# Kernel optimization log

Hardware: AMD Instinct MI355X
Metric: run time of the kernel (lower is better)

The kernel has to match this reference:

```python
import jax, jax.numpy as jnp
import numpy as np

D_MODEL = 2048
D_KV = 512
D_Q = 1536
N_HEADS = 16
HEAD_DIM = 128
ROPE_BASE = 10000.0


def apply_rope(x, past_len=0):
    # x: [B, H, S, D]; interleaved-pair rotation (pairs (2i, 2i+1))
    B, H, S, D = x.shape
    half = D // 2
    pos = (jnp.arange(S) + past_len).astype(jnp.float32)
    inv_freq = 1.0 / (ROPE_BASE ** (jnp.arange(half, dtype=jnp.float32) * 2.0 / D))
    ang = pos[:, None] * inv_freq[None, :]          # [S, half]
    cos, sin = jnp.cos(ang), jnp.sin(ang)
    x1 = x[..., 0::2]
    x2 = x[..., 1::2]
    r1 = x1 * cos - x2 * sin
    r2 = x1 * sin + x2 * cos
    return jnp.stack([r1, r2], axis=-1).reshape(x.shape)


def setup_inputs() -> dict:
    key = jax.random.key(0)
    ks = jax.random.split(key, 16)
    s = 0.02
    inp = {
        "h": jax.random.normal(ks[0], (2, 2048, D_MODEL), dtype=jnp.float32),
        # weights stored [in, out] (y = x @ W + b)
        "W_DKV": jax.random.normal(ks[1], (D_MODEL, D_KV)) * s,
        "b_DKV": jnp.zeros((D_KV,)),
        "W_UK": jax.random.normal(ks[2], (D_KV, N_HEADS * HEAD_DIM)) * s,
        "b_UK": jnp.zeros((N_HEADS * HEAD_DIM,)),
        "W_UV": jax.random.normal(ks[3], (D_KV, N_HEADS * HEAD_DIM)) * s,
        "b_UV": jnp.zeros((N_HEADS * HEAD_DIM,)),
        "W_DQ": jax.random.normal(ks[4], (D_MODEL, D_Q)) * s,
        "b_DQ": jnp.zeros((D_Q,)),
        "W_UQ": jax.random.normal(ks[5], (D_Q, N_HEADS * HEAD_DIM)) * s,
        "b_UQ": jnp.zeros((N_HEADS * HEAD_DIM,)),
        "W_KR": jax.random.normal(ks[6], (D_MODEL, D_MODEL)) * s,
        "b_KR": jnp.zeros((D_MODEL,)),
        "W_O": jax.random.normal(ks[7], (D_MODEL, D_MODEL)) * s,
        "b_O": jnp.zeros((D_MODEL,)),
    }
    return inp


def reference(h, W_DKV, b_DKV, W_UK, b_UK, W_UV, b_UV, W_DQ, b_DQ,
              W_UQ, b_UQ, W_KR, b_KR, W_O, b_O):
    B, S, _ = h.shape

    def split_heads(x):  # [B,S,H*D] -> [B,H,S,D]
        return x.reshape(B, S, N_HEADS, HEAD_DIM).transpose(0, 2, 1, 3)

    # latent KV path (prefill: no cache)
    c_KV = h @ W_DKV + b_DKV                     # [B,S,d_kv] latent cache
    k_C = split_heads(c_KV @ W_UK + b_UK)        # [B,H,S,Dh]
    v_C = split_heads(c_KV @ W_UV + b_UV)        # [B,H,S,Dh]

    # decoupled RoPE K path
    kr_cache = h @ W_KR + b_KR                   # [B,S,d_model]
    k_R = apply_rope(split_heads(kr_cache))      # [B,H,S,Dh]
    k = jnp.concatenate([k_C, k_R], axis=-1)     # [B,H,S,2*Dh]

    # latent Q path
    c_Q = h @ W_DQ + b_DQ
    q_C = split_heads(c_Q @ W_UQ + b_UQ)
    q_R = apply_rope(q_C, past_len=0)
    q = jnp.concatenate([q_C, q_R], axis=-1)     # [B,H,S,2*Dh]

    # causal attention
    scale = 1.0 / jnp.sqrt(jnp.float32(q.shape[-1]))
    scores = jnp.einsum("bhqd,bhkd->bhqk", q, k) * scale
    causal = jnp.tril(jnp.ones((S, S), dtype=bool))
    scores = jnp.where(causal, scores, jnp.finfo(scores.dtype).min)
    attn = jax.nn.softmax(scores, axis=-1)
    ctx = jnp.einsum("bhqk,bhkd->bhqd", attn, v_C)
    ctx = ctx.transpose(0, 2, 1, 3).reshape(B, S, N_HEADS * HEAD_DIM)
    out = ctx @ W_O + b_O
    return (out, c_KV, kr_cache)
```

## Files before the change

kernel.cpp:

```cpp
#include <hip/hip_runtime.h>
#include <cstdint>
#include <cstddef>

typedef __bf16 bf16;
typedef __bf16 bf16x8 __attribute__((ext_vector_type(8)));
typedef float  f32x4  __attribute__((ext_vector_type(4)));

__device__ __forceinline__ void async_copy16(const void* g, void* l)
{
    auto gp = (__attribute__((address_space(1))) const void*)(reinterpret_cast<uintptr_t>(g));
    auto lp = (__attribute__((address_space(3))) void*)(uint32_t)(reinterpret_cast<uintptr_t>(l));
    __builtin_amdgcn_global_load_lds(gp, lp, 16, 0, 0);
}

__global__ void cast_to_bf16(const float* __restrict__ in, bf16* __restrict__ out, int n)
{
    const int i = (blockIdx.x * 256 + threadIdx.x) * 4;
    if (i < n) {
        const float4 v = *(const float4*)(in + i);
        out[i]     = (bf16)v.x;
        out[i + 1] = (bf16)v.y;
        out[i + 2] = (bf16)v.z;
        out[i + 3] = (bf16)v.w;
    }
}

__global__ void transpose_cast(const float* __restrict__ in, bf16* __restrict__ out,
                               int R, int Ccols)
{
    __shared__ float tile[32][33];
    const int c0 = blockIdx.x * 32;
    const int r0 = blockIdx.y * 32;
    const int tx = threadIdx.x, ty = threadIdx.y;
    for (int i = ty; i < 32; i += 8)
        tile[i][tx] = in[(size_t)(r0 + i) * Ccols + c0 + tx];
    __syncthreads();
    for (int i = ty; i < 32; i += 8)
        out[(size_t)(c0 + i) * R + r0 + tx] = (bf16)tile[tx][i];
}

__global__ __launch_bounds__(256, 2)
void gemm_bt(const bf16* __restrict__ A, const bf16* __restrict__ Bt,
             const float* __restrict__ bias, float* __restrict__ C,
             bf16* __restrict__ Cb, int M, int N, int K)
{
    __shared__ bf16 As[128 * 64];
    __shared__ bf16 Bs[128 * 64];
    const int tid  = threadIdx.x;
    const int wave = tid >> 6;
    const int lane = tid & 63;
    const int quad = lane >> 4;
    const int l15  = lane & 15;
    const int m0   = blockIdx.y * 128;
    const int n0   = blockIdx.x * 128;
    const int wm   = (wave >> 1) * 64;
    const int wn   = (wave & 1) * 64;

    const int srow = lane >> 3;
    const int scol = (lane & 7) * 8;
    const bf16* Ab = A  + (size_t)(m0 + wave * 32 + srow) * K + scol;
    const bf16* Bb = Bt + (size_t)(n0 + wave * 32 + srow) * K + scol;
    bf16* AsW = &As[(wave * 32) * 64];
    bf16* BsW = &Bs[(wave * 32) * 64];

    f32x4 acc[4][4] = {};

    for (int k0 = 0; k0 < K; k0 += 64) {
        __syncthreads();
#pragma unroll
        for (int i = 0; i < 4; ++i) {
            async_copy16(Ab + (size_t)(i * 8) * K + k0, AsW + i * 8 * 64);
            async_copy16(Bb + (size_t)(i * 8) * K + k0, BsW + i * 8 * 64);
        }
        __syncthreads();
#pragma unroll
        for (int ks = 0; ks < 2; ++ks) {
            bf16x8 af[4], bfr[4];
#pragma unroll
            for (int i = 0; i < 4; ++i)
                af[i] = *(const bf16x8*)&As[(wm + i * 16 + l15) * 64 + ks * 32 + quad * 8];
#pragma unroll
            for (int j = 0; j < 4; ++j)
                bfr[j] = *(const bf16x8*)&Bs[(wn + j * 16 + l15) * 64 + ks * 32 + quad * 8];
#pragma unroll
            for (int i = 0; i < 4; ++i)
#pragma unroll
                for (int j = 0; j < 4; ++j)
                    acc[i][j] = __builtin_amdgcn_mfma_f32_16x16x32_bf16(af[i], bfr[j], acc[i][j], 0, 0, 0);
        }
    }

#pragma unroll
    for (int j = 0; j < 4; ++j) {
        const int col = n0 + wn + j * 16 + l15;
        const float bv = bias[col];
#pragma unroll
        for (int i = 0; i < 4; ++i) {
            const int row = m0 + wm + i * 16 + quad * 4;
#pragma unroll
            for (int r = 0; r < 4; ++r) {
                const float v = acc[i][j][r] + bv;
                if (C)  C [(size_t)(row + r) * N + col] = v;
                if (Cb) Cb[(size_t)(row + r) * N + col] = (bf16)v;
            }
        }
    }
}

__global__ void transpose_v(const bf16* __restrict__ vC, bf16* __restrict__ vT)
{
    __shared__ bf16 tile[32][33];
    const int bh = blockIdx.z, b = bh >> 4, h = bh & 15;
    const int s0 = blockIdx.x * 32, d0 = blockIdx.y * 32;
    const int tx = threadIdx.x, ty = threadIdx.y;
    for (int i = ty; i < 32; i += 8)
        tile[i][tx] = vC[((size_t)(b * 2048 + s0 + i)) * 2048 + h * 128 + d0 + tx];
    __syncthreads();
    for (int i = ty; i < 32; i += 8)
        vT[((size_t)(bh * 128 + d0 + i)) * 2048 + s0 + tx] = tile[tx][i];
}

#define INVF_C 0.20762050593046014f

template <typename T>
__global__ void rope_heads(const T* __restrict__ in, bf16* __restrict__ out)
{
    const int idx = blockIdx.x * 256 + threadIdx.x;
    const int j = idx & 63;
    const int h = (idx >> 6) & 15;
    const int s = (idx >> 10) & 2047;
    const int b = idx >> 21;
    const size_t src = ((size_t)(b * 2048 + s)) * 2048 + h * 128 + 2 * j;
    const float x1 = (float)in[src], x2 = (float)in[src + 1];
    const float ang = (float)s * exp2f(-(float)j * INVF_C);
    float sn, cs;
    sincosf(ang, &sn, &cs);
    out[src]     = (bf16)(x1 * cs - x2 * sn);
    out[src + 1] = (bf16)(x1 * sn + x2 * cs);
}

__global__ __launch_bounds__(512, 2)
void mla_attn(const bf16* __restrict__ qCp, const bf16* __restrict__ qRp,
              const bf16* __restrict__ kCp, const bf16* __restrict__ kRp,
              const bf16* __restrict__ Vt, bf16* __restrict__ ctx)
{
    __shared__ bf16 Ks[64 * 264];
    __shared__ bf16 Vs[128 * 72];
    __shared__ bf16 Ps[128 * 72];
    const int bh   = blockIdx.x;
    const int b    = bh >> 4, hh = bh & 15;
    const int yq   = blockIdx.y;
    const int qt   = (yq < 8) ? (2 * yq) : (31 - 2 * yq);
    const int q0   = qt * 128;
    const int tid  = threadIdx.x;
    const int wave = tid >> 6;
    const int lane = tid & 63;
    const int quad = lane >> 4;
    const int l15  = lane & 15;
    const int wq   = q0 + wave * 16;

    bf16x8 qf[8];
    {
        const size_t qoff = ((size_t)(b * 2048 + wq + l15)) * 2048
                          + hh * 128 + quad * 8;
#pragma unroll
        for (int ks = 0; ks < 4; ++ks) {
            qf[ks]     = *(const bf16x8*)(qCp + qoff + ks * 32);
            qf[4 + ks] = *(const bf16x8*)(qRp + qoff + ks * 32);
        }
    }

    float mstate[4], lstate[4];
    f32x4 o[8];
#pragma unroll
    for (int r = 0; r < 4; ++r) { mstate[r] = -1e30f; lstate[r] = 0.0f; }
#pragma unroll
    for (int dt = 0; dt < 8; ++dt) { f32x4 z = {0.f, 0.f, 0.f, 0.f}; o[dt] = z; }

    const int krow = tid >> 4, kcol = (tid & 15) * 8;
    const int vsr  = tid >> 3, vsc  = (tid & 7) * 8;

    const int ntiles = 2 * qt + 2;
    for (int t = 0; t < ntiles; ++t) {
        const int kk0 = t * 64;
        __syncthreads();
#pragma unroll
        for (int it = 0; it < 2; ++it) {
            const int row = it * 32 + krow;
            const size_t g = ((size_t)(b * 2048 + kk0 + row)) * 2048 + hh * 128 + kcol;
            *(bf16x8*)&Ks[row * 264 + kcol]       = *(const bf16x8*)(kCp + g);
            *(bf16x8*)&Ks[row * 264 + 128 + kcol] = *(const bf16x8*)(kRp + g);
        }
#pragma unroll
        for (int it = 0; it < 2; ++it) {
            const int d = it * 64 + vsr;
            *(bf16x8*)&Vs[d * 72 + vsc] =
                *(const bf16x8*)(Vt + ((size_t)(bh * 128 + d)) * 2048 + kk0 + vsc);
        }
        __syncthreads();

        if (kk0 <= wq + 15) {
            f32x4 sc[4] = {};
#pragma unroll
            for (int ks = 0; ks < 8; ++ks)
#pragma unroll
                for (int j = 0; j < 4; ++j) {
                    bf16x8 kf = *(const bf16x8*)&Ks[(j * 16 + l15) * 264 + ks * 32 + quad * 8];
                    sc[j] = __builtin_amdgcn_mfma_f32_16x16x32_bf16(qf[ks], kf, sc[j], 0, 0, 0);
                }

            const bool diag = (kk0 + 63 > wq);
            float rowmax[4] = {-1e30f, -1e30f, -1e30f, -1e30f};
#pragma unroll
            for (int j = 0; j < 4; ++j) {
                const int kkcol = kk0 + j * 16 + l15;
#pragma unroll
                for (int r = 0; r < 4; ++r) {
                    float s = sc[j][r] * 0.0625f;
                    if (diag && (kkcol > wq + quad * 4 + r)) s = -1e30f;
                    sc[j][r] = s;
                    rowmax[r] = fmaxf(rowmax[r], s);
                }
            }
#pragma unroll
            for (int r = 0; r < 4; ++r) {
                float v = rowmax[r];
                v = fmaxf(v, __shfl_xor(v, 1, 64));
                v = fmaxf(v, __shfl_xor(v, 2, 64));
                v = fmaxf(v, __shfl_xor(v, 4, 64));
                v = fmaxf(v, __shfl_xor(v, 8, 64));
                rowmax[r] = v;
            }
            float alpha[4];
#pragma unroll
            for (int r = 0; r < 4; ++r) {
                const float mnew = fmaxf(mstate[r], rowmax[r]);
                alpha[r] = __expf(mstate[r] - mnew);
                mstate[r] = mnew;
            }
            float rowsum[4] = {0.f, 0.f, 0.f, 0.f};
#pragma unroll
            for (int j = 0; j < 4; ++j)
#pragma unroll
                for (int r = 0; r < 4; ++r) {
                    const float p = __expf(sc[j][r] - mstate[r]);
                    sc[j][r] = p;
                    rowsum[r] += p;
                }
#pragma unroll
            for (int r = 0; r < 4; ++r) {
                float v = rowsum[r];
                v += __shfl_xor(v, 1, 64);
                v += __shfl_xor(v, 2, 64);
                v += __shfl_xor(v, 4, 64);
                v += __shfl_xor(v, 8, 64);
                lstate[r] = lstate[r] * alpha[r] + v;
            }
#pragma unroll
            for (int j = 0; j < 4; ++j)
#pragma unroll
                for (int r = 0; r < 4; ++r)
                    Ps[(wave * 16 + quad * 4 + r) * 72 + j * 16 + l15] = (bf16)sc[j][r];
#pragma unroll
            for (int dt = 0; dt < 8; ++dt)
#pragma unroll
                for (int r = 0; r < 4; ++r)
                    o[dt][r] *= alpha[r];
#pragma unroll
            for (int ks2 = 0; ks2 < 2; ++ks2) {
                bf16x8 pf = *(const bf16x8*)&Ps[(wave * 16 + l15) * 72 + ks2 * 32 + quad * 8];
#pragma unroll
                for (int dt = 0; dt < 8; ++dt) {
                    bf16x8 vf = *(const bf16x8*)&Vs[(dt * 16 + l15) * 72 + ks2 * 32 + quad * 8];
                    o[dt] = __builtin_amdgcn_mfma_f32_16x16x32_bf16(pf, vf, o[dt], 0, 0, 0);
                }
            }
        }
    }

    float inv_l[4];
#pragma unroll
    for (int r = 0; r < 4; ++r) inv_l[r] = 1.0f / lstate[r];
#pragma unroll
    for (int dt = 0; dt < 8; ++dt) {
        const int d = dt * 16 + l15;
#pragma unroll
        for (int r = 0; r < 4; ++r) {
            const int q = wq + quad * 4 + r;
            ctx[((size_t)(b * 2048 + q)) * 2048 + hh * 128 + d] = (bf16)(o[dt][r] * inv_l[r]);
        }
    }
}

extern "C" void kernel_launch(void* const* d_in, const int* in_sizes, int n_in,
                              void* d_out, int out_size, void* d_ws, size_t ws_size,
                              hipStream_t stream)
{
    const float* h     = (const float*)d_in[0];
    const float* W_DKV = (const float*)d_in[1];
    const float* b_DKV = (const float*)d_in[2];
    const float* W_UK  = (const float*)d_in[3];
    const float* b_UK  = (const float*)d_in[4];
    const float* W_UV  = (const float*)d_in[5];
    const float* b_UV  = (const float*)d_in[6];
    const float* W_DQ  = (const float*)d_in[7];
    const float* b_DQ  = (const float*)d_in[8];
    const float* W_UQ  = (const float*)d_in[9];
    const float* b_UQ  = (const float*)d_in[10];
    const float* W_KR  = (const float*)d_in[11];
    const float* b_KR  = (const float*)d_in[12];
    const float* W_O   = (const float*)d_in[13];
    const float* b_O   = (const float*)d_in[14];

    float* out   = (float*)d_out;
    float* cKV_f = out + (size_t)8388608;
    float* krc_f = out + (size_t)10485760;

    bf16* vT = (bf16*)d_out;
    bf16* qR = (bf16*)d_out + 8388608;

    bf16* ws   = (bf16*)d_ws;
    bf16* hb   = ws + 0;
    bf16* Wt   = ws + 8388608;
    bf16* cKVb = ws + 12582912;
    bf16* kC   = ws + 14680064;
    bf16* vC   = ws + 23068672;
    bf16* cQ   = ws + 31457280;
    bf16* qC   = ws + 37748736;
    bf16* kR   = hb;
    bf16* ctx  = vC;

    dim3 tb(32, 8);

    cast_to_bf16<<<8192, 256, 0, stream>>>(h, hb, 8388608);

    transpose_cast<<<dim3(16, 64), tb, 0, stream>>>(W_DKV, Wt, 2048, 512);
    gemm_bt<<<dim3(4, 32),  256, 0, stream>>>(hb, Wt, b_DKV, cKV_f, cKVb, 4096, 512,  2048);

    transpose_cast<<<dim3(64, 64), tb, 0, stream>>>(W_KR, Wt, 2048, 2048);
    gemm_bt<<<dim3(16, 32), 256, 0, stream>>>(hb, Wt, b_KR, krc_f, nullptr, 4096, 2048, 2048);

    transpose_cast<<<dim3(48, 64), tb, 0, stream>>>(W_DQ, Wt, 2048, 1536);
    gemm_bt<<<dim3(12, 32), 256, 0, stream>>>(hb, Wt, b_DQ, nullptr, cQ, 4096, 1536, 2048);

    transpose_cast<<<dim3(64, 16), tb, 0, stream>>>(W_UK, Wt, 512, 2048);
    gemm_bt<<<dim3(16, 32), 256, 0, stream>>>(cKVb, Wt, b_UK, nullptr, kC, 4096, 2048, 512);

    transpose_cast<<<dim3(64, 16), tb, 0, stream>>>(W_UV, Wt, 512, 2048);
    gemm_bt<<<dim3(16, 32), 256, 0, stream>>>(cKVb, Wt, b_UV, nullptr, vC, 4096, 2048, 512);

    transpose_cast<<<dim3(64, 48), tb, 0, stream>>>(W_UQ, Wt, 1536, 2048);
    gemm_bt<<<dim3(16, 32), 256, 0, stream>>>(cQ, Wt, b_UQ, nullptr, qC, 4096, 2048, 1536);

    rope_heads<float><<<16384, 256, 0, stream>>>(krc_f, kR);
    rope_heads<bf16 ><<<16384, 256, 0, stream>>>(qC, qR);
    transpose_v<<<dim3(64, 4, 32), tb, 0, stream>>>(vC, vT);

    mla_attn<<<dim3(32, 16), 512, 0, stream>>>(qC, qR, kC, kR, vT, ctx);

    transpose_cast<<<dim3(64, 64), tb, 0, stream>>>(W_O, Wt, 2048, 2048);
    gemm_bt<<<dim3(16, 32), 256, 0, stream>>>(ctx, Wt, b_O, out, nullptr, 4096, 2048, 2048);
}
```

Baseline: 615.2 us.

## Batch shared-input projection GEMMs and fuse Q RoPE into up-projection epilogue

Result: slower. 743.1 us (+20.8%).

```diff
diff --git a/kernel.cpp b/kernel.cpp
--- a/kernel.cpp
+++ b/kernel.cpp
@@ -5,6 +5,8 @@
 typedef __bf16 bf16;
 typedef __bf16 bf16x8 __attribute__((ext_vector_type(8)));
 typedef float  f32x4  __attribute__((ext_vector_type(4)));
+
+#define INVF_C 0.20762050593046014f
 
 __device__ __forceinline__ void async_copy16(const void* g, void* l)
 {
@@ -39,20 +41,17 @@
         out[(size_t)(c0 + i) * R + r0 + tx] = (bf16)tile[tx][i];
 }
 
-__global__ __launch_bounds__(256, 2)
-void gemm_bt(const bf16* __restrict__ A, const bf16* __restrict__ Bt,
-             const float* __restrict__ bias, float* __restrict__ C,
-             bf16* __restrict__ Cb, int M, int N, int K)
-{
-    __shared__ bf16 As[128 * 64];
-    __shared__ bf16 Bs[128 * 64];
+__device__ __forceinline__ void gemm_core(const bf16* __restrict__ A,
+                                          const bf16* __restrict__ Bt,
+                                          int K, int m0, int n0,
+                                          bf16* As, bf16* Bs,
+                                          f32x4 (&acc)[4][4])
+{
     const int tid  = threadIdx.x;
     const int wave = tid >> 6;
     const int lane = tid & 63;
     const int quad = lane >> 4;
     const int l15  = lane & 15;
-    const int m0   = blockIdx.y * 128;
-    const int n0   = blockIdx.x * 128;
     const int wm   = (wave >> 1) * 64;
     const int wn   = (wave & 1) * 64;
 
@@ -63,8 +62,6 @@
     bf16* AsW = &As[(wave * 32) * 64];
     bf16* BsW = &Bs[(wave * 32) * 64];
 
-    f32x4 acc[4][4] = {};
-
     for (int k0 = 0; k0 < K; k0 += 64) {
         __syncthreads();
 #pragma unroll
@@ -89,6 +86,27 @@
                     acc[i][j] = __builtin_amdgcn_mfma_f32_16x16x32_bf16(af[i], bfr[j], acc[i][j], 0, 0, 0);
         }
     }
+}
+
+__global__ __launch_bounds__(256, 2)
+void gemm_bt(const bf16* __restrict__ A, const bf16* __restrict__ Bt,
+             const float* __restrict__ bias, float* __restrict__ C,
+             bf16* __restrict__ Cb, int M, int N, int K)
+{
+    __shared__ bf16 As[128 * 64];
+    __shared__ bf16 Bs[128 * 64];
+    const int m0 = blockIdx.y * 128;
+    const int n0 = blockIdx.x * 128;
+    f32x4 acc[4][4] = {};
+    gemm_core(A, Bt, K, m0, n0, As, Bs, acc);
+
+    const int tid  = threadIdx.x;
+    const int wave = tid >> 6;
+    const int lane = tid & 63;
+    const int quad = lane >> 4;
+    const int l15  = lane & 15;
+    const int wm   = (wave >> 1) * 64;
+    const int wn   = (wave & 1) * 64;
 
 #pragma unroll
     for (int j = 0; j < 4; ++j) {
@@ -102,6 +120,161 @@
                 const float v = acc[i][j][r] + bv;
                 if (C)  C [(size_t)(row + r) * N + col] = v;
                 if (Cb) Cb[(size_t)(row + r) * N + col] = (bf16)v;
+            }
+        }
+    }
+}
+
+__global__ __launch_bounds__(256, 2)
+void gemm_batch1(const bf16* __restrict__ A, const bf16* __restrict__ WtAll,
+                 const float* __restrict__ bDKV, const float* __restrict__ bKR,
+                 const float* __restrict__ bDQ,
+                 float* __restrict__ cKV_f, bf16* __restrict__ cKVb,
+                 float* __restrict__ krc_f, bf16* __restrict__ cQ)
+{
+    __shared__ bf16 As[128 * 64];
+    __shared__ bf16 Bs[128 * 64];
+    const int m0 = blockIdx.y * 128;
+    const int n0 = blockIdx.x * 128;
+    f32x4 acc[4][4] = {};
+    gemm_core(A, WtAll, 2048, m0, n0, As, Bs, acc);
+
+    const int tid  = threadIdx.x;
+    const int wave = tid >> 6;
+    const int lane = tid & 63;
+    const int quad = lane >> 4;
+    const int l15  = lane & 15;
+    const int wm   = (wave >> 1) * 64;
+    const int wn   = (wave & 1) * 64;
+
+    if (n0 < 512) {
+#pragma unroll
+        for (int j = 0; j < 4; ++j) {
+            const int col = n0 + wn + j * 16 + l15;
+            const float bv = bDKV[col];
+#pragma unroll
+            for (int i = 0; i < 4; ++i) {
+                const int row = m0 + wm + i * 16 + quad * 4;
+#pragma unroll
+                for (int r = 0; r < 4; ++r) {
+                    const float v = acc[i][j][r] + bv;
+                    cKV_f[(size_t)(row + r) * 512 + col] = v;
+                    cKVb [(size_t)(row + r) * 512 + col] = (bf16)v;
+                }
+            }
+        }
+    } else if (n0 < 2560) {
+#pragma unroll
+        for (int j = 0; j < 4; ++j) {
+            const int col = n0 + wn + j * 16 + l15;
+            const int cl  = col - 512;
+            const float bv = bKR[cl];
+#pragma unroll
+            for (int i = 0; i < 4; ++i) {
+                const int row = m0 + wm + i * 16 + quad * 4;
+#pragma unroll
+                for (int r = 0; r < 4; ++r)
+                    krc_f[(size_t)(row + r) * 2048 + cl] = acc[i][j][r] + bv;
+            }
+        }
+    } else {
+#pragma unroll
+        for (int j = 0; j < 4; ++j) {
+            const int col = n0 + wn + j * 16 + l15;
+            const int cl  = col - 2560;
+            const float bv = bDQ[cl];
+#pragma unroll
+            for (int i = 0; i < 4; ++i) {
+                const int row = m0 + wm + i * 16 + quad * 4;
+#pragma unroll
+                for (int r = 0; r < 4; ++r)
+                    cQ[(size_t)(row + r) * 1536 + cl] = (bf16)(acc[i][j][r] + bv);
+            }
+        }
+    }
+}
+
+__global__ __launch_bounds__(256, 2)
+void gemm_batch45(const bf16* __restrict__ A, const bf16* __restrict__ Wt45,
+                  const float* __restrict__ bUK, const float* __restrict__ bUV,
+                  bf16* __restrict__ kC, bf16* __restrict__ vC)
+{
+    __shared__ bf16 As[128 * 64];
+    __shared__ bf16 Bs[128 * 64];
+    const int m0 = blockIdx.y * 128;
+    const int n0 = blockIdx.x * 128;
+    f32x4 acc[4][4] = {};
+    gemm_core(A, Wt45, 512, m0, n0, As, Bs, acc);
+
+    const int tid  = threadIdx.x;
+    const int wave = tid >> 6;
+    const int lane = tid & 63;
+    const int quad = lane >> 4;
+    const int l15  = lane & 15;
+    const int wm   = (wave >> 1) * 64;
+    const int wn   = (wave & 1) * 64;
+
+    const bool isK = (n0 < 2048);
+    bf16* outp = isK ? kC : vC;
+    const float* bp = isK ? bUK : bUV;
+    const int base = isK ? 0 : 2048;
+#pragma unroll
+    for (int j = 0; j < 4; ++j) {
+        const int col = n0 + wn + j * 16 + l15;
+        const int cl  = col - base;
+        const float bv = bp[cl];
+#pragma unroll
+        for (int i = 0; i < 4; ++i) {
+            const int row = m0 + wm + i * 16 + quad * 4;
+#pragma unroll
+            for (int r = 0; r < 4; ++r)
+                outp[(size_t)(row + r) * 2048 + cl] = (bf16)(acc[i][j][r] + bv);
+        }
+    }
+}
+
+__global__ __launch_bounds__(256, 2)
+void gemm_q_rope(const bf16* __restrict__ A, const bf16* __restrict__ Bt,
+                 const float* __restrict__ bias,
+                 bf16* __restrict__ qC, bf16* __restrict__ qR)
+{
+    __shared__ bf16 As[128 * 64];
+    __shared__ bf16 Bs[128 * 64];
+    const int m0 = blockIdx.y * 128;
+    const int n0 = blockIdx.x * 128;
+    f32x4 acc[4][4] = {};
+    gemm_core(A, Bt, 1536, m0, n0, As, Bs, acc);
+
+    const int tid  = threadIdx.x;
+    const int wave = tid >> 6;
+    const int lane = tid & 63;
+    const int quad = lane >> 4;
+    const int l15  = lane & 15;
+    const int wm   = (wave >> 1) * 64;
+    const int wn   = (wave & 1) * 64;
+    const int odd  = l15 & 1;
+
+#pragma unroll
+    for (int j = 0; j < 4; ++j) {
+        const int col = n0 + wn + j * 16 + l15;
+        const float bv = bias[col];
+        const float freq = exp2f(-(float)((col & 127) >> 1) * INVF_C);
+#pragma unroll
+        for (int i = 0; i < 4; ++i) {
+            const int rowb = m0 + wm + i * 16 + quad * 4;
+#pragma unroll
+            for (int r = 0; r < 4; ++r) {
+                const int row = rowb + r;
+                const float v = acc[i][j][r] + bv;
+                qC[(size_t)row * 2048 + col] = (bf16)v;
+                const float vp = __shfl_xor(v, 1, 64);
+                const float x1 = odd ? vp : v;
+                const float x2 = odd ? v  : vp;
+                const float ang = (float)(row & 2047) * freq;
+                float sn, cs;
+                sincosf(ang, &sn, &cs);
+                qR[(size_t)row * 2048 + col] =
+                    (bf16)(odd ? (x1 * sn + x2 * cs) : (x1 * cs - x2 * sn));
             }
         }
     }
@@ -120,10 +293,7 @@
         vT[((size_t)(bh * 128 + d0 + i)) * 2048 + s0 + tx] = tile[tx][i];
 }
 
-#define INVF_C 0.20762050593046014f
-
-template <typename T>
-__global__ void rope_heads(const T* __restrict__ in, bf16* __restrict__ out)
+__global__ void rope_heads_f(const float* __restrict__ in, bf16* __restrict__ out)
 {
     const int idx = blockIdx.x * 256 + threadIdx.x;
     const int j = idx & 63;
@@ -131,7 +301,7 @@
     const int s = (idx >> 10) & 2047;
     const int b = idx >> 21;
     const size_t src = ((size_t)(b * 2048 + s)) * 2048 + h * 128 + 2 * j;
-    const float x1 = (float)in[src], x2 = (float)in[src + 1];
+    const float x1 = in[src], x2 = in[src + 1];
     const float ang = (float)s * exp2f(-(float)j * INVF_C);
     float sn, cs;
     sincosf(ang, &sn, &cs);
@@ -316,48 +486,43 @@
     float* cKV_f = out + (size_t)8388608;
     float* krc_f = out + (size_t)10485760;
 
-    bf16* vT = (bf16*)d_out;
+    bf16* qC = (bf16*)d_out;
     bf16* qR = (bf16*)d_out + 8388608;
 
-    bf16* ws   = (bf16*)d_ws;
-    bf16* hb   = ws + 0;
-    bf16* Wt   = ws + 8388608;
-    bf16* cKVb = ws + 12582912;
-    bf16* kC   = ws + 14680064;
-    bf16* vC   = ws + 23068672;
-    bf16* cQ   = ws + 31457280;
-    bf16* qC   = ws + 37748736;
-    bf16* kR   = hb;
-    bf16* ctx  = vC;
+    bf16* ws    = (bf16*)d_ws;
+    bf16* hb    = ws + 0;
+    bf16* cKVb  = ws + 8388608;
+    bf16* cQ    = ws + 10485760;
+    bf16* WtAll = ws + 16777216;
+    bf16* kC    = ws + 25165824;
+    bf16* vC    = ws + 33554432;
+    bf16* kR    = hb;
+    bf16* vT    = WtAll;
+    bf16* ctx   = vC;
 
     dim3 tb(32, 8);
 
     cast_to_bf16<<<8192, 256, 0, stream>>>(h, hb, 8388608);
 
-    transpose_cast<<<dim3(16, 64), tb, 0, stream>>>(W_DKV, Wt, 2048, 512);
-    gemm_bt<<<dim3(4, 32),  256, 0, stream>>>(hb, Wt, b_DKV, cKV_f, cKVb, 4096, 512,  2048);
-
-    transpose_cast<<<dim3(64, 64), tb, 0, stream>>>(W_KR, Wt, 2048, 2048);
-    gemm_bt<<<dim3(16, 32), 256, 0, stream>>>(hb, Wt, b_KR, krc_f, nullptr, 4096, 2048, 2048);
-
-    transpose_cast<<<dim3(48, 64), tb, 0, stream>>>(W_DQ, Wt, 2048, 1536);
-    gemm_bt<<<dim3(12, 32), 256, 0, stream>>>(hb, Wt, b_DQ, nullptr, cQ, 4096, 1536, 2048);
-
-    transpose_cast<<<dim3(64, 16), tb, 0, stream>>>(W_UK, Wt, 512, 2048);
-    gemm_bt<<<dim3(16, 32), 256, 0, stream>>>(cKVb, Wt, b_UK, nullptr, kC, 4096, 2048, 512);
-
-    transpose_cast<<<dim3(64, 16), tb, 0, stream>>>(W_UV, Wt, 512, 2048);
-    gemm_bt<<<dim3(16, 32), 256, 0, stream>>>(cKVb, Wt, b_UV, nullptr, vC, 4096, 2048, 512);
-
-    transpose_cast<<<dim3(64, 48), tb, 0, stream>>>(W_UQ, Wt, 1536, 2048);
-    gemm_bt<<<dim3(16, 32), 256, 0, stream>>>(cQ, Wt, b_UQ, nullptr, qC, 4096, 2048, 1536);
-
-    rope_heads<float><<<16384, 256, 0, stream>>>(krc_f, kR);
-    rope_heads<bf16 ><<<16384, 256, 0, stream>>>(qC, qR);
+    transpose_cast<<<dim3(16, 64), tb, 0, stream>>>(W_DKV, WtAll,                 2048, 512);
+    transpose_cast<<<dim3(64, 64), tb, 0, stream>>>(W_KR,  WtAll + 1048576,       2048, 2048);
+    transpose_cast<<<dim3(48, 64), tb, 0, stream>>>(W_DQ,  WtAll + 5242880,       2048, 1536);
+
+    gemm_batch1<<<dim3(32, 32), 256, 0, stream>>>(hb, WtAll, b_DKV, b_KR, b_DQ,
+                                                  cKV_f, cKVb, krc_f, cQ);
+    rope_heads_f<<<16384, 256, 0, stream>>>(krc_f, kR);
+
+    transpose_cast<<<dim3(64, 16), tb, 0, stream>>>(W_UK, WtAll,           512, 2048);
+    transpose_cast<<<dim3(64, 16), tb, 0, stream>>>(W_UV, WtAll + 1048576, 512, 2048);
+    gemm_batch45<<<dim3(32, 32), 256, 0, stream>>>(cKVb, WtAll, b_UK, b_UV, kC, vC);
+
+    transpose_cast<<<dim3(64, 48), tb, 0, stream>>>(W_UQ, WtAll, 1536, 2048);
+    gemm_q_rope<<<dim3(16, 32), 256, 0, stream>>>(cQ, WtAll, b_UQ, qC, qR);
+
     transpose_v<<<dim3(64, 4, 32), tb, 0, stream>>>(vC, vT);
 
     mla_attn<<<dim3(32, 16), 512, 0, stream>>>(qC, qR, kC, kR, vT, ctx);
 
-    transpose_cast<<<dim3(64, 64), tb, 0, stream>>>(W_O, Wt, 2048, 2048);
-    gemm_bt<<<dim3(16, 32), 256, 0, stream>>>(ctx, Wt, b_O, out, nullptr, 4096, 2048, 2048);
-}
+    transpose_cast<<<dim3(64, 64), tb, 0, stream>>>(W_O, WtAll, 2048, 2048);
+    gemm_bt<<<dim3(16, 32), 256, 0, stream>>>(ctx, WtAll, b_O, out, nullptr, 4096, 2048, 2048);
+}
```
